# Kernel tuning notes

Measured on AMD Instinct MI355X. Metric: run time of the kernel, lower is better.

The kernel has to match this reference:

```python
import jax, jax.numpy as jnp
import numpy as np

N, D, T = 8192, 512, 12
EPS = 1e-6


def _ln(x, g, b):
    m = jnp.mean(x, axis=-1, keepdims=True)
    v = jnp.mean((x - m) ** 2, axis=-1, keepdims=True)
    return (x - m) / jnp.sqrt(v + EPS) * g + b


def _cross(x1, x2, Wa, ba, Wb, bb, d1, d2):
    # attn_weights2: [N, N], softmax over dim=1 (rows)
    aw2 = jax.nn.softmax((x1 @ Wa.T + ba) @ x2.T, axis=1)
    fused_x2 = (aw2 @ x2) / jnp.sqrt(jnp.float32(d2))
    aw1 = jax.nn.softmax((x2 @ Wb.T + bb) @ x1.T, axis=1)
    fused_x1 = (aw1 @ x1) / jnp.sqrt(jnp.float32(d1))
    return fused_x1, fused_x2


def setup_inputs() -> dict:
    key = jax.random.key(0)
    ks = jax.random.split(key, 16)
    s = 1.0 / np.sqrt(D)
    inp = {
        'xp': jax.random.normal(ks[0], (N, D), jnp.float32),
        'xm': jax.random.normal(ks[1], (N, D), jnp.float32),
        'xs': jax.random.normal(ks[2], (N, D), jnp.float32),
        'ln_g': jnp.ones((D,), jnp.float32),
        'ln_b': jnp.zeros((D,), jnp.float32),
        # mol cross-attention: linear1 (D->D), linear2 (D->D)
        'W1': jax.random.uniform(ks[3], (D, D), jnp.float32, -s, s),
        'b1': jnp.zeros((D,), jnp.float32),
        'W2': jax.random.uniform(ks[4], (D, D), jnp.float32, -s, s),
        'b2': jnp.zeros((D,), jnp.float32),
        # smile cross-attention
        'W3': jax.random.uniform(ks[5], (D, D), jnp.float32, -s, s),
        'b3': jnp.zeros((D,), jnp.float32),
        'W4': jax.random.uniform(ks[6], (D, D), jnp.float32, -s, s),
        'b4': jnp.zeros((D,), jnp.float32),
        # pred head: 2D -> T
        'Wp': jax.random.uniform(ks[7], (T, 2 * D), jnp.float32, -1.0 / np.sqrt(2 * D), 1.0 / np.sqrt(2 * D)),
        'bp': jnp.zeros((T,), jnp.float32),
        # gate
        't': jnp.full((1,), 0.5, jnp.float32),
        'Wt1': jax.random.uniform(ks[8], (50, 1), jnp.float32, -1.0, 1.0),
        'bt1': jnp.zeros((50,), jnp.float32),
        'Wt2': jax.random.uniform(ks[9], (1, 50), jnp.float32, -1.0 / np.sqrt(50), 1.0 / np.sqrt(50)),
        'bt2': jnp.zeros((1,), jnp.float32),
    }
    return inp


def reference(xp, xm, xs, ln_g, ln_b, W1, b1, W2, b2, W3, b3, W4, b4, Wp, bp, t, Wt1, bt1, Wt2, bt2):
    x1 = _ln(xp, ln_g, ln_b)
    x2 = _ln(xm, ln_g, ln_b)
    x3 = x1  # protein encoded twice with same LayerNorm
    x4 = _ln(xs, ln_g, ln_b)

    f1, f2 = _cross(x1, x2, W1, b1, W2, b2, D, D)
    h12 = jnp.concatenate([f1 + x1, f2 + x2], axis=1)          # [N, 2D]
    out12 = jax.nn.relu(h12) @ Wp.T + bp                        # [N, T]

    f3, f4 = _cross(x3, x4, W3, b3, W4, b4, D, D)
    h34 = jnp.concatenate([f3 + x3, f4 + x4], axis=1)
    out34 = jax.nn.relu(h34) @ Wp.T + bp

    t1 = t @ Wt1.T + bt1                                        # [50]
    t2 = jax.nn.sigmoid(t1 @ Wt2.T + bt2)                       # [1]
    return t2 * out12 + (1.0 - t2) * out34
```

## Files before the change

kernel.cpp:

```cpp
#include <hip/hip_runtime.h>
#include <stdint.h>


#define DEV __device__ __forceinline__
typedef unsigned short u16;
typedef __bf16 bf16x8 __attribute__((ext_vector_type(8)));
typedef float f32x4 __attribute__((ext_vector_type(4)));

constexpr int NR = 8192;
constexpr int DDIM = 512;
constexpr int TOUT = 12;

DEV u16 f2b(float f) {
  uint32_t u = __builtin_bit_cast(uint32_t, f);
  u += 0x7fffu + ((u >> 16) & 1u);
  return (u16)(u >> 16);
}
DEV float b2f(u16 h) {
  uint32_t u = ((uint32_t)h) << 16;
  return __builtin_bit_cast(float, u);
}

__global__ __launch_bounds__(64) void ln_kernel(
    const float* __restrict__ xp, const float* __restrict__ xm,
    const float* __restrict__ xs, const float* __restrict__ g,
    const float* __restrict__ b, u16* __restrict__ o1, u16* __restrict__ o2,
    u16* __restrict__ o4) {
  int row = blockIdx.x;
  int which = blockIdx.y;
  const float* x = which == 0 ? xp : (which == 1 ? xm : xs);
  u16* o = which == 0 ? o1 : (which == 1 ? o2 : o4);
  int lane = threadIdx.x;
  const float4* xr = (const float4*)(x + (size_t)row * DDIM);
  float4 v0 = xr[lane * 2], v1 = xr[lane * 2 + 1];
  float vals[8] = {v0.x, v0.y, v0.z, v0.w, v1.x, v1.y, v1.z, v1.w};
  float s = 0.f, s2 = 0.f;
  for (int j = 0; j < 8; j++) { s += vals[j]; s2 += vals[j] * vals[j]; }
  for (int off = 1; off < 64; off <<= 1) {
    s += __shfl_xor(s, off);
    s2 += __shfl_xor(s2, off);
  }
  float m = s * (1.0f / DDIM);
  float var = s2 * (1.0f / DDIM) - m * m;
  var = fmaxf(var, 0.f);
  float rs = rsqrtf(var + 1e-6f);
  int d0 = lane * 8;
  u16 us[8];
  for (int j = 0; j < 8; j++)
    us[j] = f2b((vals[j] - m) * rs * g[d0 + j] + b[d0 + j]);
  uint4 pk;
  pk.x = (uint32_t)us[0] | ((uint32_t)us[1] << 16);
  pk.y = (uint32_t)us[2] | ((uint32_t)us[3] << 16);
  pk.z = (uint32_t)us[4] | ((uint32_t)us[5] << 16);
  pk.w = (uint32_t)us[6] | ((uint32_t)us[7] << 16);
  *(uint4*)(o + (size_t)row * DDIM + d0) = pk;
}

__global__ __launch_bounds__(256) void wconv_kernel(
    const float* __restrict__ W1, const float* __restrict__ W2,
    const float* __restrict__ W3, const float* __restrict__ W4,
    u16* __restrict__ Wb) {
  int wi = blockIdx.y;
  const float* W = wi == 0 ? W1 : (wi == 1 ? W2 : (wi == 2 ? W3 : W4));
  size_t base = ((size_t)blockIdx.x * 256 + threadIdx.x) * 8;
  const float4* src = (const float4*)(W + base);
  float4 a = src[0], c = src[1];
  float vals[8] = {a.x, a.y, a.z, a.w, c.x, c.y, c.z, c.w};
  u16 us[8];
  for (int j = 0; j < 8; j++) us[j] = f2b(vals[j]);
  uint4 pk;
  pk.x = (uint32_t)us[0] | ((uint32_t)us[1] << 16);
  pk.y = (uint32_t)us[2] | ((uint32_t)us[3] << 16);
  pk.z = (uint32_t)us[4] | ((uint32_t)us[5] << 16);
  pk.w = (uint32_t)us[6] | ((uint32_t)us[7] << 16);
  *(uint4*)(Wb + (size_t)wi * DDIM * DDIM + base) = pk;
}

__global__ __launch_bounds__(256) void transpose_kernel(
    const u16* __restrict__ s1, const u16* __restrict__ s2,
    const u16* __restrict__ s4, u16* __restrict__ t1, u16* __restrict__ t2,
    u16* __restrict__ t4) {
  constexpr int LD = 66;
  __shared__ u16 tile[64 * LD];
  int which = blockIdx.z;
  const u16* src = which == 0 ? s1 : (which == 1 ? s2 : s4);
  u16* dst = which == 0 ? t1 : (which == 1 ? t2 : t4);
  int c0 = blockIdx.x * 64;
  int r0 = blockIdx.y * 64;
  int tid = threadIdx.x;
  for (int c = tid; c < 512; c += 256) {
    int i = c >> 3, j8 = (c & 7) * 8;
    uint4 v = *(const uint4*)(src + (size_t)(r0 + i) * DDIM + c0 + j8);
    uint32_t* dw = (uint32_t*)&tile[i * LD + j8];
    dw[0] = v.x; dw[1] = v.y; dw[2] = v.z; dw[3] = v.w;
  }
  __syncthreads();
  for (int rep = 0; rep < 2; rep++) {
    int idx = rep * 256 + tid;
    int o = idx >> 3, j8 = (idx & 7) * 8;
    u16 us[8];
    for (int k = 0; k < 8; k++) us[k] = tile[(j8 + k) * LD + o];
    uint4 pk;
    pk.x = (uint32_t)us[0] | ((uint32_t)us[1] << 16);
    pk.y = (uint32_t)us[2] | ((uint32_t)us[3] << 16);
    pk.z = (uint32_t)us[4] | ((uint32_t)us[5] << 16);
    pk.w = (uint32_t)us[6] | ((uint32_t)us[7] << 16);
    *(uint4*)(dst + (size_t)(c0 + o) * NR + r0 + j8) = pk;
  }
}

template <int MODE>
DEV void gemm_core(const u16* __restrict__ A, const u16* __restrict__ B,
                   u16* __restrict__ C, const float* __restrict__ bias,
                   u16* lds, int K, int lda, int ldb, int ldc, int bx,
                   int by) {
  constexpr int TM = 4, TN = 4;
  int tid = threadIdx.x;
  int w = tid >> 6, lane = tid & 63;
  int q = lane >> 4, c16 = lane & 15;
  int n0 = bx * 128, m0 = by * 128;
  int wrow = (w >> 1) * 64, wcol = (w & 1) * 64;

  const u16* gptr[4];
  int lof[4];
#pragma unroll
  for (int j = 0; j < 4; j++) {
    int call = w + j * 4;
    bool isA = call < 8;
    int ci = isA ? call : call - 8;
    int chunk = ci * 64 + lane;
    int row = chunk >> 2;
    int gch = ((chunk & 3) - (row >> 1)) & 3;
    gptr[j] = isA ? (A + (size_t)(m0 + row) * lda + gch * 8)
                  : (B + (size_t)(n0 + row) * ldb + gch * 8);
    lof[j] = (isA ? 0 : 4096) + ci * 512;
  }
  auto stageAll = [&](int buf) {
    int bo = buf * 8192;
#pragma unroll
    for (int j = 0; j < 4; j++) {
      __builtin_amdgcn_global_load_lds(
          (const __attribute__((address_space(1))) void*)gptr[j],
          (__attribute__((address_space(3))) void*)(lds + bo + lof[j]), 16, 0,
          0);
      gptr[j] += 32;
    }
  };

  f32x4 acc[TM][TN] = {};
  int nk = K >> 5;
  stageAll(0);
  stageAll(1);
  for (int ks = 0; ks < nk; ks++) {
    int cur = ks & 1;
    if (ks + 1 < nk)
      asm volatile("s_waitcnt vmcnt(4)" ::: "memory");
    else
      asm volatile("s_waitcnt vmcnt(0)" ::: "memory");
    __builtin_amdgcn_sched_barrier(0);
    __builtin_amdgcn_s_barrier();
    __builtin_amdgcn_sched_barrier(0);
    const u16* Asm = lds + cur * 8192;
    const u16* Bsm = Asm + 4096;
    bf16x8 af[TM], bfr[TN];
#pragma unroll
    for (int i = 0; i < TM; i++) {
      int r = wrow + i * 16 + c16;
      af[i] = *(const bf16x8*)&Asm[r * 32 + (((q + (r >> 1)) & 3) * 8)];
    }
#pragma unroll
    for (int n = 0; n < TN; n++) {
      int r = wcol + n * 16 + c16;
      bfr[n] = *(const bf16x8*)&Bsm[r * 32 + (((q + (r >> 1)) & 3) * 8)];
    }
    __builtin_amdgcn_s_setprio(1);
#pragma unroll
    for (int i = 0; i < TM; i++)
#pragma unroll
      for (int n = 0; n < TN; n++)
        acc[i][n] = __builtin_amdgcn_mfma_f32_16x16x32_bf16(af[i], bfr[n],
                                                            acc[i][n], 0, 0, 0);
    __builtin_amdgcn_s_setprio(0);
    asm volatile("s_waitcnt lgkmcnt(0)" ::: "memory");
    __builtin_amdgcn_sched_barrier(0);
    __builtin_amdgcn_s_barrier();
    __builtin_amdgcn_sched_barrier(0);
    if (ks + 2 < nk) stageAll(cur);
  }
  for (int h = 0; h < 2; h++) {
    __syncthreads();
    if ((w & 1) == h) {
      for (int i = 0; i < TM; i++) {
        for (int n = 0; n < TN; n++) {
          float bv = 0.f;
          if constexpr (MODE == 0) bv = bias[n0 + wcol + n * 16 + c16];
          for (int r = 0; r < 4; r++) {
            int rl = wrow + i * 16 + q * 4 + r;
            int cl = (n * 16 + c16) ^ ((rl & 7) << 3);
            float v = acc[i][n][r];
            if constexpr (MODE == 0) v += bv;
            if constexpr (MODE == 1) v = __expf(v - 48.0f);
            lds[rl * 64 + cl] = f2b(v);
          }
        }
      }
    }
    __syncthreads();
    for (int rep = 0; rep < 4; rep++) {
      int idx = rep * 256 + tid;
      int row = idx >> 3, seg = idx & 7;
      uint4 vv = ((const uint4*)lds)[row * 8 + (seg ^ (row & 7))];
      *(uint4*)(C + (size_t)(m0 + row) * ldc + n0 + h * 64 + seg * 8) = vv;
    }
  }
}

DEV void pv_body(const u16* __restrict__ A, const u16* __restrict__ B,
                 u16* lds, u16* __restrict__ C, int bx, int by) {
  constexpr int BM = 64, BN = 128, BK = 64;
  int tid = threadIdx.x, w = tid >> 6, lane = tid & 63;
  int q = lane >> 4, c16 = lane & 15;
  int n0 = bx * BN, m0 = by * BM;
  int wr = (w >> 1) * 32, wc = (w & 1) * 64;
  f32x4 acc[2][4] = {};
  f32x4 accl[2] = {};
  bf16x8 ones;
  for (int j = 0; j < 8; j++) ones[j] = (__bf16)1.0f;

  const u16* gptr[6];
  int lof0[6], lof1[6];
#pragma unroll
  for (int it = 0; it < 6; it++) {
    int cb = it * 256 + w * 64;
    int c = cb + lane;
    bool isA = cb < 512;
    int ci = isA ? c : c - 512;
    int row = ci >> 3;
    int koff = ((ci & 7) ^ (row & 7)) * 8;
    gptr[it] = isA ? (A + (size_t)(m0 + row) * NR + koff)
                   : (B + (size_t)(n0 + row) * NR + koff);
    lof0[it] = isA ? (cb * 8) : (8192 + (cb - 512) * 8);
    lof1[it] = isA ? (4096 + cb * 8) : (16384 + (cb - 512) * 8);
  }
  auto stage = [&](int buf) {
#pragma unroll
    for (int it = 0; it < 6; it++) {
      int lo = buf ? lof1[it] : lof0[it];
      __builtin_amdgcn_global_load_lds(
          (const __attribute__((address_space(1))) void*)gptr[it],
          (__attribute__((address_space(3))) void*)(lds + lo), 16, 0, 0);
      gptr[it] += BK;
    }
  };

  constexpr int KSTEPS = NR / BK;
  stage(0);
  stage(1);
  for (int ks = 0; ks < KSTEPS; ks++) {
    int cur = ks & 1;
    if (ks + 1 < KSTEPS)
      asm volatile("s_waitcnt vmcnt(6)" ::: "memory");
    else
      asm volatile("s_waitcnt vmcnt(0)" ::: "memory");
    __builtin_amdgcn_sched_barrier(0);
    __builtin_amdgcn_s_barrier();
    __builtin_amdgcn_sched_barrier(0);
    const u16* Asm = lds + cur * 4096;
    const u16* Bsm = lds + 8192 + cur * 8192;
#pragma unroll
    for (int kh = 0; kh < 2; kh++) {
      bf16x8 af[2], bfr[4];
      int cl = kh * 4 + q;
#pragma unroll
      for (int i = 0; i < 2; i++) {
        int r = wr + i * 16 + c16;
        af[i] = *(const bf16x8*)&Asm[r * BK + ((cl ^ (r & 7)) * 8)];
      }
#pragma unroll
      for (int n = 0; n < 4; n++) {
        int r = wc + n * 16 + c16;
        bfr[n] = *(const bf16x8*)&Bsm[r * BK + ((cl ^ (r & 7)) * 8)];
      }
      __builtin_amdgcn_s_setprio(1);
#pragma unroll
      for (int i = 0; i < 2; i++)
        accl[i] = __builtin_amdgcn_mfma_f32_16x16x32_bf16(af[i], ones, accl[i],
                                                          0, 0, 0);
#pragma unroll
      for (int i = 0; i < 2; i++)
#pragma unroll
        for (int n = 0; n < 4; n++)
          acc[i][n] = __builtin_amdgcn_mfma_f32_16x16x32_bf16(
              af[i], bfr[n], acc[i][n], 0, 0, 0);
      __builtin_amdgcn_s_setprio(0);
    }
    asm volatile("s_waitcnt lgkmcnt(0)" ::: "memory");
    __builtin_amdgcn_sched_barrier(0);
    __builtin_amdgcn_s_barrier();
    __builtin_amdgcn_sched_barrier(0);
    if (ks + 2 < KSTEPS) stage(cur);
  }
  for (int i = 0; i < 2; i++) {
    float invl[4];
    for (int r = 0; r < 4; r++)
      invl[r] = 0.044194173824159216f / accl[i][r];
    for (int n = 0; n < 4; n++) {
      int col = n0 + wc + n * 16 + c16;
      for (int r = 0; r < 4; r++) {
        int row = m0 + wr + i * 16 + q * 4 + r;
        C[(size_t)row * DDIM + col] = f2b(acc[i][n][r] * invl[r]);
      }
    }
  }
}

DEV void pv_remap(int bid, int& bx, int& by) {
  bx = (bid >> 3) & 3;
  by = (bid & 7) + 8 * (bid >> 5);
}

__global__ __launch_bounds__(256, 4) void scores_kernel(
    const u16* __restrict__ Q, const u16* __restrict__ Kv,
    u16* __restrict__ P) {
  __shared__ u16 lds[16384];
  gemm_core<1>(Q, Kv, P, nullptr, lds, DDIM, DDIM, DDIM, NR, blockIdx.x,
               blockIdx.y);
}

__global__ __launch_bounds__(256, 4) void qproj_kernel(
    const u16* __restrict__ s0, const u16* __restrict__ s1,
    const u16* __restrict__ s2, const u16* __restrict__ s3,
    const u16* __restrict__ Wb, const float* __restrict__ b0,
    const float* __restrict__ b1, const float* __restrict__ b2,
    const float* __restrict__ b3, u16* __restrict__ Qs) {
  __shared__ u16 lds[16384];
  int z = blockIdx.z;
  const u16* A = z == 0 ? s0 : (z == 1 ? s1 : (z == 2 ? s2 : s3));
  const float* bias = z == 0 ? b0 : (z == 1 ? b1 : (z == 2 ? b2 : b3));
  gemm_core<0>(A, Wb + (size_t)z * DDIM * DDIM, Qs + (size_t)z * NR * DDIM,
               bias, lds, DDIM, DDIM, DDIM, DDIM, blockIdx.x, blockIdx.y);
}

__global__ __launch_bounds__(256, 4) void qscombo_kernel(
    const u16* __restrict__ x1b, const u16* __restrict__ x2b,
    const u16* __restrict__ x4b, const u16* __restrict__ Wb,
    const float* __restrict__ b1, const float* __restrict__ b2,
    const float* __restrict__ b3, u16* __restrict__ Qs,
    const u16* __restrict__ Q0, u16* __restrict__ P) {
  __shared__ u16 lds[16384];
  if (blockIdx.x < 768) {
    int b = blockIdx.x;
    int z = 1 + (b >> 8), rem = b & 255;
    const u16* A = z == 1 ? x2b : (z == 2 ? x1b : x4b);
    const float* bias = z == 1 ? b1 : (z == 2 ? b2 : b3);
    gemm_core<0>(A, Wb + (size_t)z * DDIM * DDIM, Qs + (size_t)z * NR * DDIM,
                 bias, lds, DDIM, DDIM, DDIM, DDIM, rem & 3, rem >> 2);
  } else {
    int b = blockIdx.x - 768;
    gemm_core<1>(Q0, x2b, P, nullptr, lds, DDIM, DDIM, DDIM, NR, b & 63,
                 b >> 6);
  }
}

__global__ __launch_bounds__(256, 3) void pv_kernel(
    const u16* __restrict__ A, const u16* __restrict__ B,
    u16* __restrict__ C) {
  __shared__ u16 lds[24576];
  int bx, by;
  pv_remap(blockIdx.x, bx, by);
  pv_body(A, B, lds, C, bx, by);
}

__global__ __launch_bounds__(256, 3) void combo_kernel(
    const u16* __restrict__ Pin, const u16* __restrict__ Vt,
    u16* __restrict__ F, const u16* __restrict__ Q,
    const u16* __restrict__ Kv, u16* __restrict__ Pout) {
  __shared__ u16 lds[24576];
  if (blockIdx.x < 512) {
    int bx, by;
    pv_remap(blockIdx.x, bx, by);
    pv_body(Pin, Vt, lds, F, bx, by);
  } else {
    int b = blockIdx.x - 512;
    gemm_core<1>(Q, Kv, Pout, nullptr, lds, DDIM, DDIM, DDIM, NR, b & 63,
                 b >> 6);
  }
}

__global__ __launch_bounds__(256) void head_kernel(
    const u16* __restrict__ F1, const u16* __restrict__ F2,
    const u16* __restrict__ F3, const u16* __restrict__ F4,
    const u16* __restrict__ x1, const u16* __restrict__ x2,
    const u16* __restrict__ x4, const float* __restrict__ Wp,
    const float* __restrict__ bp, const float* __restrict__ tg,
    const float* __restrict__ Wt1, const float* __restrict__ bt1,
    const float* __restrict__ Wt2, const float* __restrict__ bt2,
    float* __restrict__ out) {
  __shared__ float wps[TOUT * 2 * DDIM];
  __shared__ float t2s;
  int tid = threadIdx.x;
  for (int i = tid; i < TOUT * 2 * DDIM; i += 256) wps[i] = Wp[i];
  if (tid == 0) {
    float s = bt2[0];
    for (int k = 0; k < 50; k++) s += Wt2[k] * (tg[0] * Wt1[k] + bt1[k]);
    t2s = 1.0f / (1.0f + __expf(-s));
  }
  __syncthreads();
  int g = tid >> 5, j = tid & 31;
  size_t m = (size_t)blockIdx.x * 8 + g;
  float a12[TOUT] = {}, a34[TOUT] = {};
  for (int d = j; d < 2 * DDIM; d += 32) {
    float h12, h34;
    if (d < DDIM) {
      float xv = b2f(x1[m * DDIM + d]);
      h12 = b2f(F1[m * DDIM + d]) + xv;
      h34 = b2f(F3[m * DDIM + d]) + xv;
    } else {
      int dd = d - DDIM;
      h12 = b2f(F2[m * DDIM + dd]) + b2f(x2[m * DDIM + dd]);
      h34 = b2f(F4[m * DDIM + dd]) + b2f(x4[m * DDIM + dd]);
    }
    h12 = fmaxf(h12, 0.f);
    h34 = fmaxf(h34, 0.f);
    for (int t = 0; t < TOUT; t++) {
      float wv = wps[t * 2 * DDIM + d];
      a12[t] += h12 * wv;
      a34[t] += h34 * wv;
    }
  }
  for (int off = 1; off < 32; off <<= 1)
    for (int t = 0; t < TOUT; t++) {
      a12[t] += __shfl_xor(a12[t], off);
      a34[t] += __shfl_xor(a34[t], off);
    }
  if (j < TOUT) {
    float t2 = t2s;
    out[m * TOUT + j] = t2 * a12[j] + (1.f - t2) * a34[j] + bp[j];
  }
}

extern "C" void kernel_launch(void* const* d_in, const int* in_sizes, int n_in,
                              void* d_out, int out_size, void* d_ws,
                              size_t ws_size, hipStream_t stream) {
  (void)in_sizes; (void)n_in; (void)out_size;
  const float* xp = (const float*)d_in[0];
  const float* xm = (const float*)d_in[1];
  const float* xs = (const float*)d_in[2];
  const float* ln_g = (const float*)d_in[3];
  const float* ln_b = (const float*)d_in[4];
  const float* Wmat[4] = {(const float*)d_in[5], (const float*)d_in[7],
                          (const float*)d_in[9], (const float*)d_in[11]};
  const float* bvec[4] = {(const float*)d_in[6], (const float*)d_in[8],
                          (const float*)d_in[10], (const float*)d_in[12]};
  const float* Wp = (const float*)d_in[13];
  const float* bp = (const float*)d_in[14];
  const float* tg = (const float*)d_in[15];
  const float* Wt1 = (const float*)d_in[16];
  const float* bt1 = (const float*)d_in[17];
  const float* Wt2 = (const float*)d_in[18];
  const float* bt2 = (const float*)d_in[19];
  float* out = (float*)d_out;

  char* ws = (char*)d_ws;
  const size_t MB = 1ull << 20;
  u16* x1b = (u16*)(ws + 0 * MB);
  u16* x2b = (u16*)(ws + 8 * MB);
  u16* x4b = (u16*)(ws + 16 * MB);
  u16* x1t = (u16*)(ws + 24 * MB);
  u16* x2t = (u16*)(ws + 32 * MB);
  u16* x4t = (u16*)(ws + 40 * MB);
  u16* Wb = (u16*)(ws + 48 * MB);
  u16* Qs = (u16*)(ws + 52 * MB);
  u16* P0 = (u16*)(ws + 84 * MB);
  bool dual = ws_size >= 340 * MB;
  u16* P1 = dual ? (u16*)(ws + 212 * MB) : P0;

  ln_kernel<<<dim3(NR, 3), 64, 0, stream>>>(xp, xm, xs, ln_g, ln_b, x1b, x2b,
                                            x4b);
  wconv_kernel<<<dim3(128, 4), 256, 0, stream>>>(Wmat[0], Wmat[1], Wmat[2],
                                                 Wmat[3], Wb);
  transpose_kernel<<<dim3(8, 128, 3), 256, 0, stream>>>(x1b, x2b, x4b, x1t,
                                                        x2t, x4t);
  qproj_kernel<<<dim3(DDIM / 128, NR / 128, 1), 256, 0, stream>>>(
      x1b, x2b, x1b, x4b, Wb, bvec[0], bvec[1], bvec[2], bvec[3], Qs);

  const u16* kvb[4] = {x2b, x1b, x4b, x1b};
  const u16* kvt[4] = {x2t, x1t, x4t, x1t};
  u16* slot[4];
  for (int a = 0; a < 4; a++) slot[a] = Qs + (size_t)a * NR * DDIM;

  qscombo_kernel<<<dim3(768 + 64 * 64), 256, 0, stream>>>(
      x1b, x2b, x4b, Wb, bvec[1], bvec[2], bvec[3], Qs, slot[0], P0);

  if (dual) {
    u16* Pb[4] = {P0, P1, P0, P1};
    for (int a = 0; a < 3; a++) {
      combo_kernel<<<dim3(512 + 64 * 64), 256, 0, stream>>>(
          Pb[a], kvt[a], slot[a], slot[a + 1], kvb[a + 1], Pb[a + 1]);
    }
    pv_kernel<<<dim3(512), 256, 0, stream>>>(Pb[3], kvt[3], slot[3]);
  } else {
    for (int a = 0; a < 4; a++) {
      if (a > 0)
        scores_kernel<<<dim3(64, 64), 256, 0, stream>>>(slot[a], kvb[a], P0);
      pv_kernel<<<dim3(512), 256, 0, stream>>>(P0, kvt[a], slot[a]);
    }
  }

  head_kernel<<<dim3(NR / 8), 256, 0, stream>>>(
      slot[1], slot[0], slot[3], slot[2], x1b, x2b, x4b, Wp, bp, tg, Wt1, bt1,
      Wt2, bt2, out);
}
```

Measured before the change: 901.0 us.

## Enlarge GEMM tile to 256x128 and remap score blocks for L2 locality

```diff
diff --git a/kernel.cpp b/kernel.cpp
--- a/kernel.cpp
+++ b/kernel.cpp
@@ -114,31 +114,31 @@
                    u16* __restrict__ C, const float* __restrict__ bias,
                    u16* lds, int K, int lda, int ldb, int ldc, int bx,
                    int by) {
-  constexpr int TM = 4, TN = 4;
+  constexpr int TM = 8, TN = 4;
   int tid = threadIdx.x;
   int w = tid >> 6, lane = tid & 63;
   int q = lane >> 4, c16 = lane & 15;
-  int n0 = bx * 128, m0 = by * 128;
-  int wrow = (w >> 1) * 64, wcol = (w & 1) * 64;
-
-  const u16* gptr[4];
-  int lof[4];
-#pragma unroll
-  for (int j = 0; j < 4; j++) {
-    int call = w + j * 4;
-    bool isA = call < 8;
-    int ci = isA ? call : call - 8;
-    int chunk = ci * 64 + lane;
-    int row = chunk >> 2;
-    int gch = ((chunk & 3) - (row >> 1)) & 3;
+  int n0 = bx * 128, m0 = by * 256;
+  int wrow = (w >> 1) * 128, wcol = (w & 1) * 64;
+
+  const u16* gptr[6];
+  int lof[6];
+#pragma unroll
+  for (int j = 0; j < 6; j++) {
+    int cb = j * 256 + w * 64;
+    int c = cb + lane;
+    bool isA = cb < 1024;
+    int ci = isA ? c : c - 1024;
+    int row = ci >> 2;
+    int gch = ((ci & 3) - (row >> 1)) & 3;
     gptr[j] = isA ? (A + (size_t)(m0 + row) * lda + gch * 8)
                   : (B + (size_t)(n0 + row) * ldb + gch * 8);
-    lof[j] = (isA ? 0 : 4096) + ci * 512;
+    lof[j] = isA ? (cb * 8) : (8192 + (cb - 1024) * 8);
   }
   auto stageAll = [&](int buf) {
-    int bo = buf * 8192;
-#pragma unroll
-    for (int j = 0; j < 4; j++) {
+    int bo = buf * 12288;
+#pragma unroll
+    for (int j = 0; j < 6; j++) {
       __builtin_amdgcn_global_load_lds(
           (const __attribute__((address_space(1))) void*)gptr[j],
           (__attribute__((address_space(3))) void*)(lds + bo + lof[j]), 16, 0,
@@ -154,14 +154,14 @@
   for (int ks = 0; ks < nk; ks++) {
     int cur = ks & 1;
     if (ks + 1 < nk)
-      asm volatile("s_waitcnt vmcnt(4)" ::: "memory");
+      asm volatile("s_waitcnt vmcnt(6)" ::: "memory");
     else
       asm volatile("s_waitcnt vmcnt(0)" ::: "memory");
     __builtin_amdgcn_sched_barrier(0);
     __builtin_amdgcn_s_barrier();
     __builtin_amdgcn_sched_barrier(0);
-    const u16* Asm = lds + cur * 8192;
-    const u16* Bsm = Asm + 4096;
+    const u16* Asm = lds + cur * 12288;
+    const u16* Bsm = Asm + 8192;
     bf16x8 af[TM], bfr[TN];
 #pragma unroll
     for (int i = 0; i < TM; i++) {
@@ -206,7 +206,7 @@
       }
     }
     __syncthreads();
-    for (int rep = 0; rep < 4; rep++) {
+    for (int rep = 0; rep < 8; rep++) {
       int idx = rep * 256 + tid;
       int row = idx >> 3, seg = idx & 7;
       uint4 vv = ((const uint4*)lds)[row * 8 + (seg ^ (row & 7))];
@@ -319,21 +319,28 @@
   by = (bid & 7) + 8 * (bid >> 5);
 }
 
-__global__ __launch_bounds__(256, 4) void scores_kernel(
+DEV void scores_remap(int sb, int& bx, int& by) {
+  int L = (sb & 7) * 256 + (sb >> 3);
+  bx = L & 63;
+  by = L >> 6;
+}
+
+__global__ __launch_bounds__(256, 2) void scores_kernel(
     const u16* __restrict__ Q, const u16* __restrict__ Kv,
     u16* __restrict__ P) {
-  __shared__ u16 lds[16384];
-  gemm_core<1>(Q, Kv, P, nullptr, lds, DDIM, DDIM, DDIM, NR, blockIdx.x,
-               blockIdx.y);
-}
-
-__global__ __launch_bounds__(256, 4) void qproj_kernel(
+  __shared__ u16 lds[24576];
+  int bx, by;
+  scores_remap(blockIdx.x, bx, by);
+  gemm_core<1>(Q, Kv, P, nullptr, lds, DDIM, DDIM, DDIM, NR, bx, by);
+}
+
+__global__ __launch_bounds__(256, 2) void qproj_kernel(
     const u16* __restrict__ s0, const u16* __restrict__ s1,
     const u16* __restrict__ s2, const u16* __restrict__ s3,
     const u16* __restrict__ Wb, const float* __restrict__ b0,
     const float* __restrict__ b1, const float* __restrict__ b2,
     const float* __restrict__ b3, u16* __restrict__ Qs) {
-  __shared__ u16 lds[16384];
+  __shared__ u16 lds[24576];
   int z = blockIdx.z;
   const u16* A = z == 0 ? s0 : (z == 1 ? s1 : (z == 2 ? s2 : s3));
   const float* bias = z == 0 ? b0 : (z == 1 ? b1 : (z == 2 ? b2 : b3));
@@ -341,24 +348,25 @@
                bias, lds, DDIM, DDIM, DDIM, DDIM, blockIdx.x, blockIdx.y);
 }
 
-__global__ __launch_bounds__(256, 4) void qscombo_kernel(
+__global__ __launch_bounds__(256, 2) void qscombo_kernel(
     const u16* __restrict__ x1b, const u16* __restrict__ x2b,
     const u16* __restrict__ x4b, const u16* __restrict__ Wb,
     const float* __restrict__ b1, const float* __restrict__ b2,
     const float* __restrict__ b3, u16* __restrict__ Qs,
     const u16* __restrict__ Q0, u16* __restrict__ P) {
-  __shared__ u16 lds[16384];
-  if (blockIdx.x < 768) {
+  __shared__ u16 lds[24576];
+  if (blockIdx.x < 384) {
     int b = blockIdx.x;
-    int z = 1 + (b >> 8), rem = b & 255;
+    int z = 1 + (b >> 7), rem = b & 127;
     const u16* A = z == 1 ? x2b : (z == 2 ? x1b : x4b);
     const float* bias = z == 1 ? b1 : (z == 2 ? b2 : b3);
     gemm_core<0>(A, Wb + (size_t)z * DDIM * DDIM, Qs + (size_t)z * NR * DDIM,
                  bias, lds, DDIM, DDIM, DDIM, DDIM, rem & 3, rem >> 2);
   } else {
-    int b = blockIdx.x - 768;
-    gemm_core<1>(Q0, x2b, P, nullptr, lds, DDIM, DDIM, DDIM, NR, b & 63,
-                 b >> 6);
+    int sb = blockIdx.x - 384;
+    int bx, by;
+    scores_remap(sb, bx, by);
+    gemm_core<1>(Q0, x2b, P, nullptr, lds, DDIM, DDIM, DDIM, NR, bx, by);
   }
 }
 
@@ -371,7 +379,7 @@
   pv_body(A, B, lds, C, bx, by);
 }
 
-__global__ __launch_bounds__(256, 3) void combo_kernel(
+__global__ __launch_bounds__(256, 2) void combo_kernel(
     const u16* __restrict__ Pin, const u16* __restrict__ Vt,
     u16* __restrict__ F, const u16* __restrict__ Q,
     const u16* __restrict__ Kv, u16* __restrict__ Pout) {
@@ -381,9 +389,10 @@
     pv_remap(blockIdx.x, bx, by);
     pv_body(Pin, Vt, lds, F, bx, by);
   } else {
-    int b = blockIdx.x - 512;
-    gemm_core<1>(Q, Kv, Pout, nullptr, lds, DDIM, DDIM, DDIM, NR, b & 63,
-                 b >> 6);
+    int sb = blockIdx.x - 512;
+    int bx, by;
+    scores_remap(sb, bx, by);
+    gemm_core<1>(Q, Kv, Pout, nullptr, lds, DDIM, DDIM, DDIM, NR, bx, by);
   }
 }
 
@@ -481,7 +490,7 @@
                                                  Wmat[3], Wb);
   transpose_kernel<<<dim3(8, 128, 3), 256, 0, stream>>>(x1b, x2b, x4b, x1t,
                                                         x2t, x4t);
-  qproj_kernel<<<dim3(DDIM / 128, NR / 128, 1), 256, 0, stream>>>(
+  qproj_kernel<<<dim3(4, 32, 1), 256, 0, stream>>>(
       x1b, x2b, x1b, x4b, Wb, bvec[0], bvec[1], bvec[2], bvec[3], Qs);
 
   const u16* kvb[4] = {x2b, x1b, x4b, x1b};
@@ -489,20 +498,20 @@
   u16* slot[4];
   for (int a = 0; a < 4; a++) slot[a] = Qs + (size_t)a * NR * DDIM;
 
-  qscombo_kernel<<<dim3(768 + 64 * 64), 256, 0, stream>>>(
+  qscombo_kernel<<<dim3(384 + 2048), 256, 0, stream>>>(
       x1b, x2b, x4b, Wb, bvec[1], bvec[2], bvec[3], Qs, slot[0], P0);
 
   if (dual) {
     u16* Pb[4] = {P0, P1, P0, P1};
     for (int a = 0; a < 3; a++) {
-      combo_kernel<<<dim3(512 + 64 * 64), 256, 0, stream>>>(
+      combo_kernel<<<dim3(512 + 2048), 256, 0, stream>>>(
           Pb[a], kvt[a], slot[a], slot[a + 1], kvb[a + 1], Pb[a + 1]);
     }
     pv_kernel<<<dim3(512), 256, 0, stream>>>(Pb[3], kvt[3], slot[3]);
   } else {
     for (int a = 0; a < 4; a++) {
       if (a > 0)
-        scores_kernel<<<dim3(64, 64), 256, 0, stream>>>(slot[a], kvb[a], P0);
+        scores_kernel<<<dim3(2048), 256, 0, stream>>>(slot[a], kvb[a], P0);
       pv_kernel<<<dim3(512), 256, 0, stream>>>(P0, kvt[a], slot[a]);
     }
   }
```

Result: slower. 1.007 ms (+11.8%).
